# Kernel tuning notes

Hardware: AMD Instinct MI355X
Metric: run time of the kernel (lower is better)

The kernel has to match this reference:

```python
import jax, jax.numpy as jnp
import numpy as np

INPUT_DIM = 64
HIDDEN = 256
BATCH = 256
SEQ = 512
LN_EPS = 1e-5


def setup_inputs() -> dict:
    key = jax.random.key(0)
    ks = jax.random.split(key, 10)
    def lin(k, fan_in, fan_out):
        bound = 1.0 / np.sqrt(fan_in)
        kw, kb = jax.random.split(k)
        W = jax.random.uniform(kw, (fan_in, fan_out), jnp.float32, -bound, bound)
        b = jax.random.uniform(kb, (fan_out,), jnp.float32, -bound, bound)
        return W, b
    x = jax.random.normal(ks[0], (BATCH, SEQ, INPUT_DIM), jnp.float32)
    # layer 0: input_dim -> hidden
    Wz0, bz0 = lin(ks[1], INPUT_DIM + HIDDEN, 3 * HIDDEN)
    Wc0, bc0 = lin(ks[2], INPUT_DIM + HIDDEN, HIDDEN)
    # layer 1: hidden -> hidden
    Wz1, bz1 = lin(ks[3], HIDDEN + HIDDEN, 3 * HIDDEN)
    Wc1, bc1 = lin(ks[4], HIDDEN + HIDDEN, HIDDEN)
    ln_gamma = jnp.ones((HIDDEN,), jnp.float32)
    ln_beta = jnp.zeros((HIDDEN,), jnp.float32)
    return {"x": x, "Wz0": Wz0, "bz0": bz0, "Wc0": Wc0, "bc0": bc0,
            "Wz1": Wz1, "bz1": bz1, "Wc1": Wc1, "bc1": bc1,
            "ln_gamma": ln_gamma, "ln_beta": ln_beta}


def _gru_cell(h, x_t, Wz, bz, Wc, bc):
    # combined = [h, x]  (hidden first, as in the torch code)
    combined = jnp.concatenate([h, x_t], axis=-1)
    gates = combined @ Wz + bz  # (B, 3H); third chunk is unused (as in source)
    z = jax.nn.sigmoid(gates[:, :HIDDEN])
    r = jax.nn.sigmoid(gates[:, HIDDEN:2 * HIDDEN])
    reset_combined = jnp.concatenate([r * h, x_t], axis=-1)
    h_tilde = jnp.tanh(reset_combined @ Wc + bc)
    return (1.0 - z) * h + z * h_tilde


def reference(x, Wz0, bz0, Wc0, bc0, Wz1, bz1, Wc1, bc1, ln_gamma, ln_beta):
    # sanitize: NaN -> 0, Inf -> sign * 10
    x = jnp.where(jnp.isnan(x), 0.0, x)
    x = jnp.where(jnp.isinf(x), jnp.sign(x) * 10.0, x)

    B = x.shape[0]
    h0 = jnp.zeros((B, HIDDEN), x.dtype)
    h1 = jnp.zeros((B, HIDDEN), x.dtype)

    def step(carry, x_t):
        h0, h1 = carry
        h0 = _gru_cell(h0, x_t, Wz0, bz0, Wc0, bc0)
        h1 = _gru_cell(h1, h0, Wz1, bz1, Wc1, bc1)
        return (h0, h1), None

    xs = jnp.swapaxes(x, 0, 1)  # (seq, batch, input_dim)
    (h0, h1), _ = jax.lax.scan(step, (h0, h1), xs)

    # LayerNorm on final top-layer hidden state
    mean = jnp.mean(h1, axis=-1, keepdims=True)
    var = jnp.var(h1, axis=-1, keepdims=True)
    enc = (h1 - mean) * jax.lax.rsqrt(var + LN_EPS) * ln_gamma + ln_beta
    return enc
```

## Files before the change

kernel.cpp:

```cpp
#include <hip/hip_runtime.h>


#define SEQL 512
#define CH 8
#define NCH 64
#define DEPTH 4

#define RB0  1310720u
#define GSTR 1048576u
#define CTRB (RB0 + 16u * GSTR)

typedef __bf16 bf16x8 __attribute__((ext_vector_type(8)));
typedef float f32x4 __attribute__((ext_vector_type(4)));
typedef unsigned int u32x4 __attribute__((ext_vector_type(4)));
typedef unsigned long long u64;

__device__ __forceinline__ unsigned short f2bf(float f) {
  unsigned int u = __builtin_bit_cast(unsigned int, f);
  u += 0x7fffu + ((u >> 16) & 1u);
  return (unsigned short)(u >> 16);
}
__device__ __forceinline__ float bf2f(unsigned short u) {
  unsigned int v = ((unsigned int)u) << 16;
  return __builtin_bit_cast(float, v);
}
__device__ __forceinline__ float sigm(float x) { return 1.0f / (1.0f + __expf(-x)); }
__device__ __forceinline__ float tanh_(float x) { return 1.0f - 2.0f / (__expf(2.0f * x) + 1.0f); }
__device__ __forceinline__ float sanit(float v) {
  if (!(v == v)) return 0.f;
  if (isinf(v)) return v > 0.f ? 10.f : -10.f;
  return v;
}

__device__ __forceinline__ void st8(u64* p, u64 v) {
  __hip_atomic_store(p, v, __ATOMIC_RELAXED, __HIP_MEMORY_SCOPE_AGENT);
}

__device__ __forceinline__ void ld_frame8(const unsigned short* base, int lane, u32x4* c) {
  const char* p0 = (const char*)base + lane * 16;
  const char* p4 = p0 + 4096;
  asm volatile(
      "global_load_dwordx4 %0, %8, off sc0 sc1\n\t"
      "global_load_dwordx4 %1, %8, off offset:1024 sc0 sc1\n\t"
      "global_load_dwordx4 %2, %8, off offset:2048 sc0 sc1\n\t"
      "global_load_dwordx4 %3, %8, off offset:3072 sc0 sc1\n\t"
      "global_load_dwordx4 %4, %9, off sc0 sc1\n\t"
      "global_load_dwordx4 %5, %9, off offset:1024 sc0 sc1\n\t"
      "global_load_dwordx4 %6, %9, off offset:2048 sc0 sc1\n\t"
      "global_load_dwordx4 %7, %9, off offset:3072 sc0 sc1\n\t"
      "s_waitcnt vmcnt(0)"
      : "=&v"(c[0]), "=&v"(c[1]), "=&v"(c[2]), "=&v"(c[3]),
        "=&v"(c[4]), "=&v"(c[5]), "=&v"(c[6]), "=&v"(c[7])
      : "v"(p0), "v"(p4)
      : "memory");
}
__device__ __forceinline__ void ld_part6(const unsigned short* pf, int wave, int lane,
                                         u64* z, u64* r, u64* c) {
  const char* p0 = (const char*)pf + ((2 * wave) * 64 + lane) * 8;
  const char* p1 = p0 + 8192;
  const char* p2 = p0 + 16384;
  asm volatile(
      "global_load_dwordx2 %0, %6, off sc0 sc1\n\t"
      "global_load_dwordx2 %1, %6, off offset:512 sc0 sc1\n\t"
      "global_load_dwordx2 %2, %7, off sc0 sc1\n\t"
      "global_load_dwordx2 %3, %7, off offset:512 sc0 sc1\n\t"
      "global_load_dwordx2 %4, %8, off sc0 sc1\n\t"
      "global_load_dwordx2 %5, %8, off offset:512 sc0 sc1\n\t"
      "s_waitcnt vmcnt(0)"
      : "=&v"(z[0]), "=&v"(z[1]), "=&v"(r[0]), "=&v"(r[1]),
        "=&v"(c[0]), "=&v"(c[1])
      : "v"(p0), "v"(p1), "v"(p2)
      : "memory");
}

__global__ __launch_bounds__(256) void prep_weights(
    const float* __restrict__ Wz0, const float* __restrict__ Wc0,
    const float* __restrict__ Wz1, const float* __restrict__ Wc1,
    unsigned short* __restrict__ ws) {
  int idx = blockIdx.x * 256 + threadIdx.x;
  const float* W;
  int stride, KT, base;
  if (idx < 163840)      { W = Wz0; stride = 768; KT = 10; base = 0; }
  else if (idx < 245760) { W = Wc0; stride = 256; KT = 10; base = 163840; idx -= 163840; }
  else if (idx < 507904) { W = Wz1; stride = 768; KT = 16; base = 245760; idx -= 245760; }
  else                   { W = Wc1; stride = 256; KT = 16; base = 507904; idx -= 507904; }
  int tile = idx >> 9;
  int t = idx & 511;
  int nt = tile / KT;
  int kt = tile - nt * KT;
  int n15 = t & 15;
  int klocal = t >> 4;
  int k = (kt << 5) + klocal;
  int n = (nt << 4) + n15;
  int lane = ((klocal >> 3) << 4) | n15;
  int j = klocal & 7;
  ws[base + (tile << 9) + (lane << 3) + j] = f2bf(W[k * stride + n]);
}

__device__ __forceinline__ void waitge(int* p, int v, int tid) {
  __syncthreads();
  if (tid == 0) {
    long it = 0;
    while (__hip_atomic_load(p, __ATOMIC_RELAXED, __HIP_MEMORY_SCOPE_AGENT) < v) {
      __builtin_amdgcn_s_sleep(1);
      if (++it > (1L << 24)) break;
    }
  }
  __syncthreads();
}
__device__ __forceinline__ void publish(int* p, int v, int tid) {
  asm volatile("s_waitcnt vmcnt(0)" ::: "memory");
  __syncthreads();
  if (tid == 0) __hip_atomic_store(p, v, __ATOMIC_RELAXED, __HIP_MEMORY_SCOPE_AGENT);
}

#define DLOC(c) ((((c) >> 5) << 9) + (((((c) >> 3) & 3) << 4) + (quad << 2)) * 8 + ((c) & 7))
#define MFMA(a, b, c) __builtin_amdgcn_mfma_f32_16x16x32_bf16((a), (b), (c), 0, 0, 0)

union UB  { u32x4 q; bf16x8 v; };
union UB8 { u64 q; ushort4 s; };

__global__ __launch_bounds__(512, 2) void gru_pipe(
    const float* __restrict__ x,
    const float* __restrict__ bz0, const float* __restrict__ bc0,
    const float* __restrict__ bz1, const float* __restrict__ bc1,
    const float* __restrict__ gamma, const float* __restrict__ beta,
    const unsigned short* __restrict__ wsw,
    unsigned short* __restrict__ gws,
    float* __restrict__ out) {
  __shared__ __align__(16) unsigned short lds[75776];
  const int tid  = threadIdx.x;
  const int wave = tid >> 6;
  const int lane = tid & 63;
  const int l15  = lane & 15;
  const int quad = lane >> 4;
  const int stage = blockIdx.x >> 4;
  const int g     = blockIdx.x & 15;
  const int row0  = g << 4;

  const bf16x8* __restrict__ wsv = (const bf16x8*)wsw;
  unsigned short* ringh = gws + (RB0 >> 1) + (size_t)g * (GSTR >> 1);
  unsigned short* ringp = ringh + 131072;
  int* ctr = (int*)((char*)gws + CTRB) + g * 16;

  if (stage == 0) {
    unsigned short* h0f  = lds;
    unsigned short* rh0f = lds + 4096;
    unsigned short* xf   = lds + 8192;
    unsigned short* xw   = lds + 10240;
    unsigned short* cw0  = lds + 59392;
    for (int u = tid; u < 6144; u += 512) {
      int flat = u << 3, ti = flat >> 9, q = flat & 511, srct;
      if (ti < 64) srct = (ti >> 1) * 10 + 8 + (ti & 1);
      else         srct = 320 + ((ti - 64) >> 1) * 10 + 8 + (ti & 1);
      *(uint4*)(xw + flat) = *(const uint4*)(wsw + srct * 512 + q);
    }
    for (int u = tid; u < 2048; u += 512) {
      int flat = u << 3, ti = flat >> 9, q = flat & 511;
      int srct = 320 + (ti >> 1) * 10 + 6 + (ti & 1);
      *(uint4*)(cw0 + flat) = *(const uint4*)(wsw + srct * 512 + q);
    }
    for (int i = tid; i < 4096; i += 512) h0f[i] = 0;

    bf16x8 pz[2][8], pr[2][8], pc[2][6];
#pragma unroll
    for (int j = 0; j < 2; ++j) {
      const int zt = 2 * wave + j;
#pragma unroll
      for (int k = 0; k < 8; ++k) {
        pz[j][k] = wsv[(zt * 10 + k) * 64 + lane];
        pr[j][k] = wsv[((16 + zt) * 10 + k) * 64 + lane];
      }
#pragma unroll
      for (int k = 0; k < 6; ++k)
        pc[j][k] = wsv[(320 + zt * 10 + k) * 64 + lane];
    }
#pragma unroll
    for (int j = 0; j < 2; ++j) {
#pragma unroll
      for (int k = 0; k < 8; ++k)
        asm volatile("" : "+a"(pz[j][k]), "+a"(pr[j][k]));
#pragma unroll
      for (int k = 0; k < 6; ++k)
        asm volatile("" : "+a"(pc[j][k]));
    }

    float bzz[2], bzr[2], bcc[2];
    int dloc[2];
#pragma unroll
    for (int j = 0; j < 2; ++j) {
      const int col = 32 * wave + 16 * j + l15;
      bzz[j] = bz0[col]; bzr[j] = bz0[256 + col]; bcc[j] = bc0[col];
      dloc[j] = DLOC(col);
    }
    f32x4 h0s[2] = {{0,0,0,0},{0,0,0,0}};

    const int xrow = (tid >> 4) & 15, c4 = (tid & 15) << 2;
    const float* xp = x + (size_t)(row0 + xrow) * (SEQL * 64) + c4;
    const int xbase = ((c4 >> 5) << 9) + ((((c4 >> 3) & 3) << 4) + xrow) * 8 + (c4 & 7);
    if (tid < 256) {
      float4 xv = *(const float4*)xp;
      xf[xbase] = f2bf(sanit(xv.x)); xf[xbase + 1] = f2bf(sanit(xv.y));
      xf[xbase + 2] = f2bf(sanit(xv.z)); xf[xbase + 3] = f2bf(sanit(xv.w));
    }
    __syncthreads();

    for (int ch = 0; ch < NCH; ++ch) {
      if (ch >= DEPTH) waitge(ctr + 2, ch - (DEPTH - 1), tid);
      unsigned short* slot = ringh + (ch & (DEPTH - 1)) * (CH * 4096);
      for (int s = 0; s < CH; ++s) {
        const int t = (ch << 3) + s;
        if (s > 0) {
          u64* dst = (u64*)(slot + (s - 1) * 4096);
          const u64* src = (const u64*)h0f;
#pragma unroll
          for (int q = 0; q < 2; ++q) st8(dst + tid + 512 * q, src[tid + 512 * q]);
        }
        const unsigned short* xb = xf + ((t & 1) << 10);
        const bool havex = (t + 1 < SEQL) && (tid < 256);
        float4 xn;
        if (havex) xn = *(const float4*)(xp + (t + 1) * 64);

        f32x4 za[2], ra[2];
#pragma unroll
        for (int j = 0; j < 2; ++j) { za[j] = {bzz[j],bzz[j],bzz[j],bzz[j]}; ra[j] = {bzr[j],bzr[j],bzr[j],bzr[j]}; }
#pragma unroll
        for (int k = 0; k < 8; ++k) {
          bf16x8 a = *(const bf16x8*)(h0f + (k << 9) + (lane << 3));
#pragma unroll
          for (int j = 0; j < 2; ++j) { za[j] = MFMA(a, pz[j][k], za[j]); ra[j] = MFMA(a, pr[j][k], ra[j]); }
        }
#pragma unroll
        for (int k = 0; k < 2; ++k) {
          bf16x8 a = *(const bf16x8*)(xb + (k << 9) + (lane << 3));
#pragma unroll
          for (int j = 0; j < 2; ++j) {
            bf16x8 bz_ = *(const bf16x8*)(xw + ((((2 * wave + j) << 1) | k) << 9) + (lane << 3));
            bf16x8 br_ = *(const bf16x8*)(xw + ((((16 + 2 * wave + j) << 1) | k) << 9) + (lane << 3));
            za[j] = MFMA(a, bz_, za[j]); ra[j] = MFMA(a, br_, ra[j]);
          }
        }
        float zg[2][4];
#pragma unroll
        for (int j = 0; j < 2; ++j)
#pragma unroll
          for (int i = 0; i < 4; ++i) {
            zg[j][i] = sigm(za[j][i]);
            rh0f[dloc[j] + i * 8] = f2bf(sigm(ra[j][i]) * h0s[j][i]);
          }
        __syncthreads();

        f32x4 ca[2];
#pragma unroll
        for (int j = 0; j < 2; ++j) ca[j] = {bcc[j],bcc[j],bcc[j],bcc[j]};
#pragma unroll
        for (int k = 0; k < 6; ++k) {
          bf16x8 a = *(const bf16x8*)(rh0f + (k << 9) + (lane << 3));
#pragma unroll
          for (int j = 0; j < 2; ++j) ca[j] = MFMA(a, pc[j][k], ca[j]);
        }
#pragma unroll
        for (int kk = 0; kk < 2; ++kk) {
          bf16x8 a = *(const bf16x8*)(rh0f + ((6 + kk) << 9) + (lane << 3));
#pragma unroll
          for (int j = 0; j < 2; ++j) {
            bf16x8 bc_ = *(const bf16x8*)(cw0 + ((((2 * wave + j) << 1) | kk) << 9) + (lane << 3));
            ca[j] = MFMA(a, bc_, ca[j]);
          }
        }
#pragma unroll
        for (int k = 0; k < 2; ++k) {
          bf16x8 a = *(const bf16x8*)(xb + (k << 9) + (lane << 3));
#pragma unroll
          for (int j = 0; j < 2; ++j) {
            bf16x8 bc_ = *(const bf16x8*)(xw + 32768 + ((((2 * wave + j) << 1) | k) << 9) + (lane << 3));
            ca[j] = MFMA(a, bc_, ca[j]);
          }
        }
#pragma unroll
        for (int j = 0; j < 2; ++j)
#pragma unroll
          for (int i = 0; i < 4; ++i) {
            float ht = tanh_(ca[j][i]);
            float hn = h0s[j][i] + zg[j][i] * (ht - h0s[j][i]);
            h0s[j][i] = hn;
            h0f[dloc[j] + i * 8] = f2bf(hn);
          }
        if (havex) {
          unsigned short* xb1 = xf + (((t + 1) & 1) << 10);
          xb1[xbase] = f2bf(sanit(xn.x)); xb1[xbase + 1] = f2bf(sanit(xn.y));
          xb1[xbase + 2] = f2bf(sanit(xn.z)); xb1[xbase + 3] = f2bf(sanit(xn.w));
        }
        __syncthreads();
      }
      {
        u64* dst = (u64*)(slot + 7 * 4096);
        const u64* src = (const u64*)h0f;
#pragma unroll
        for (int q = 0; q < 2; ++q) st8(dst + tid + 512 * q, src[tid + 512 * q]);
      }
      publish(ctr + 0, ch + 1, tid);
    }
  } else if (stage == 1) {
    unsigned short* cwB = lds;
    for (int u = tid; u < 2048; u += 512) {
      int flat = u << 3, ti = flat >> 9, q = flat & 511;
      int srct = 992 + (ti >> 1) * 16 + 14 + (ti & 1);
      *(uint4*)(cwB + flat) = *(const uint4*)(wsw + srct * 512 + q);
    }
    __syncthreads();

    bf16x8 p1[2][8], p2[2][8], p3[2][6];
#pragma unroll
    for (int j = 0; j < 2; ++j) {
      const int nt = 2 * wave + j;
#pragma unroll
      for (int k = 0; k < 8; ++k) {
        p1[j][k] = wsv[(480 + nt * 16 + 8 + k) * 64 + lane];
        p2[j][k] = wsv[(480 + (16 + nt) * 16 + 8 + k) * 64 + lane];
      }
#pragma unroll
      for (int k = 0; k < 6; ++k)
        p3[j][k] = wsv[(992 + nt * 16 + 8 + k) * 64 + lane];
    }
#pragma unroll
    for (int j = 0; j < 2; ++j) {
#pragma unroll
      for (int k = 0; k < 8; ++k)
        asm volatile("" : "+a"(p1[j][k]), "+a"(p2[j][k]));
#pragma unroll
      for (int k = 0; k < 6; ++k)
        asm volatile("" : "+a"(p3[j][k]));
    }
    float b1[2], b2[2], b3[2];
#pragma unroll
    for (int j = 0; j < 2; ++j) {
      const int col = 32 * wave + 16 * j + l15;
      b1[j] = bz1[col]; b2[j] = bz1[256 + col]; b3[j] = bc1[col];
    }
    for (int ch = 0; ch < NCH; ++ch) {
      waitge(ctr + 0, ch + 1, tid);
      if (ch >= DEPTH) waitge(ctr + 3, ch - (DEPTH - 1), tid);
      const unsigned short* hslot = ringh + (ch & (DEPTH - 1)) * (CH * 4096);
      unsigned short* pslot = ringp + (ch & (DEPTH - 1)) * (CH * 12288);
      for (int s = 0; s < CH; ++s) {
        u32x4 cf[8];
        ld_frame8(hslot + s * 4096, lane, cf);
        f32x4 za[2] = {{0,0,0,0},{0,0,0,0}};
        f32x4 ra[2] = {{0,0,0,0},{0,0,0,0}};
        f32x4 ca[2] = {{0,0,0,0},{0,0,0,0}};
#pragma unroll
        for (int k = 0; k < 8; ++k) {
          UB ub; ub.q = cf[k];
          bf16x8 a = ub.v;
#pragma unroll
          for (int j = 0; j < 2; ++j) {
            za[j] = MFMA(a, p1[j][k], za[j]);
            ra[j] = MFMA(a, p2[j][k], ra[j]);
            if (k < 6) ca[j] = MFMA(a, p3[j][k], ca[j]);
          }
        }
#pragma unroll
        for (int kk = 0; kk < 2; ++kk) {
          UB ub; ub.q = cf[6 + kk];
          bf16x8 a = ub.v;
#pragma unroll
          for (int j = 0; j < 2; ++j) {
            bf16x8 bc_ = *(const bf16x8*)(cwB + ((((2 * wave + j) << 1) | kk) << 9) + (lane << 3));
            ca[j] = MFMA(a, bc_, ca[j]);
          }
        }
        u64* pf = (u64*)(pslot + s * 12288);
#pragma unroll
        for (int j = 0; j < 2; ++j) {
          ushort4 vz, vr, vc;
          vz.x = f2bf(za[j][0] + b1[j]); vz.y = f2bf(za[j][1] + b1[j]);
          vz.z = f2bf(za[j][2] + b1[j]); vz.w = f2bf(za[j][3] + b1[j]);
          vr.x = f2bf(ra[j][0] + b2[j]); vr.y = f2bf(ra[j][1] + b2[j]);
          vr.z = f2bf(ra[j][2] + b2[j]); vr.w = f2bf(ra[j][3] + b2[j]);
          vc.x = f2bf(ca[j][0] + b3[j]); vc.y = f2bf(ca[j][1] + b3[j]);
          vc.z = f2bf(ca[j][2] + b3[j]); vc.w = f2bf(ca[j][3] + b3[j]);
          st8(pf + (2 * wave + j) * 64 + lane,      __builtin_bit_cast(u64, vz));
          st8(pf + (16 + 2 * wave + j) * 64 + lane, __builtin_bit_cast(u64, vr));
          st8(pf + (32 + 2 * wave + j) * 64 + lane, __builtin_bit_cast(u64, vc));
        }
      }
      publish(ctr + 1, ch + 1, tid);
      if (tid == 0)
        __hip_atomic_store(ctr + 2, ch + 1, __ATOMIC_RELAXED, __HIP_MEMORY_SCOPE_AGENT);
    }
  } else {
    unsigned short* h1f  = lds;
    unsigned short* rh1f = lds + 4096;
    unsigned short* cwC  = lds + 8192;
    for (int u = tid; u < 2048; u += 512) {
      int flat = u << 3, ti = flat >> 9, q = flat & 511;
      int srct = 992 + (ti >> 1) * 16 + 6 + (ti & 1);
      *(uint4*)(cwC + flat) = *(const uint4*)(wsw + srct * 512 + q);
    }
    bf16x8 q1[2][8], q2[2][8], q3[2][6];
#pragma unroll
    for (int j = 0; j < 2; ++j) {
      const int nt = 2 * wave + j;
#pragma unroll
      for (int k = 0; k < 8; ++k) {
        q1[j][k] = wsv[(480 + nt * 16 + k) * 64 + lane];
        q2[j][k] = wsv[(480 + (16 + nt) * 16 + k) * 64 + lane];
      }
#pragma unroll
      for (int k = 0; k < 6; ++k)
        q3[j][k] = wsv[(992 + nt * 16 + k) * 64 + lane];
    }
#pragma unroll
    for (int j = 0; j < 2; ++j) {
#pragma unroll
      for (int k = 0; k < 8; ++k)
        asm volatile("" : "+a"(q1[j][k]), "+a"(q2[j][k]));
#pragma unroll
      for (int k = 0; k < 6; ++k)
        asm volatile("" : "+a"(q3[j][k]));
    }
    for (int i = tid; i < 4096; i += 512) h1f[i] = 0;
    int dloc[2];
#pragma unroll
    for (int j = 0; j < 2; ++j) dloc[j] = DLOC(32 * wave + 16 * j + l15);
    f32x4 h1s[2] = {{0,0,0,0},{0,0,0,0}};
    __syncthreads();

    for (int ch = 0; ch < NCH; ++ch) {
      waitge(ctr + 1, ch + 1, tid);
      const unsigned short* pslot = ringp + (ch & (DEPTH - 1)) * (CH * 12288);
      for (int s = 0; s < CH; ++s) {
        u64 zq[2], rq[2], cq[2];
        ld_part6(pslot + s * 12288, wave, lane, zq, rq, cq);
        f32x4 za[2] = {{0,0,0,0},{0,0,0,0}};
        f32x4 ra[2] = {{0,0,0,0},{0,0,0,0}};
#pragma unroll
        for (int k = 0; k < 8; ++k) {
          bf16x8 a = *(const bf16x8*)(h1f + (k << 9) + (lane << 3));
#pragma unroll
          for (int j = 0; j < 2; ++j) { za[j] = MFMA(a, q1[j][k], za[j]); ra[j] = MFMA(a, q2[j][k], ra[j]); }
        }
        float zg[2][4];
#pragma unroll
        for (int j = 0; j < 2; ++j) {
          UB8 uz, ur; uz.q = zq[j]; ur.q = rq[j];
#pragma unroll
          for (int i = 0; i < 4; ++i) {
            zg[j][i] = sigm(za[j][i] + bf2f(((const unsigned short*)&uz.s)[i]));
            float r = sigm(ra[j][i] + bf2f(((const unsigned short*)&ur.s)[i]));
            rh1f[dloc[j] + i * 8] = f2bf(r * h1s[j][i]);
          }
        }
        __syncthreads();

        f32x4 ca[2] = {{0,0,0,0},{0,0,0,0}};
#pragma unroll
        for (int k = 0; k < 6; ++k) {
          bf16x8 a = *(const bf16x8*)(rh1f + (k << 9) + (lane << 3));
#pragma unroll
          for (int j = 0; j < 2; ++j) ca[j] = MFMA(a, q3[j][k], ca[j]);
        }
#pragma unroll
        for (int kk = 0; kk < 2; ++kk) {
          bf16x8 a = *(const bf16x8*)(rh1f + ((6 + kk) << 9) + (lane << 3));
#pragma unroll
          for (int j = 0; j < 2; ++j) {
            bf16x8 bc_ = *(const bf16x8*)(cwC + ((((2 * wave + j) << 1) | kk) << 9) + (lane << 3));
            ca[j] = MFMA(a, bc_, ca[j]);
          }
        }
#pragma unroll
        for (int j = 0; j < 2; ++j) {
          UB8 uc; uc.q = cq[j];
#pragma unroll
          for (int i = 0; i < 4; ++i) {
            float ht = tanh_(ca[j][i] + bf2f(((const unsigned short*)&uc.s)[i]));
            float hn = h1s[j][i] + zg[j][i] * (ht - h1s[j][i]);
            h1s[j][i] = hn;
            h1f[dloc[j] + i * 8] = f2bf(hn);
          }
        }
        __syncthreads();
      }
      publish(ctr + 3, ch + 1, tid);
    }

    float* h1buf = (float*)lds;
#pragma unroll
    for (int j = 0; j < 2; ++j)
#pragma unroll
      for (int i = 0; i < 4; ++i)
        h1buf[(quad * 4 + i) * 256 + 32 * wave + 16 * j + l15] = h1s[j][i];
    __syncthreads();

    if (tid < 256) {
      const int r = tid >> 4, cl = tid & 15;
      float v[16], s = 0.f, sq = 0.f;
#pragma unroll
      for (int jj = 0; jj < 16; ++jj) {
        v[jj] = h1buf[r * 256 + cl + (jj << 4)];
        s += v[jj]; sq += v[jj] * v[jj];
      }
#pragma unroll
      for (int off = 8; off > 0; off >>= 1) {
        s  += __shfl_xor(s, off);
        sq += __shfl_xor(sq, off);
      }
      const float mean = s * (1.f / 256.f);
      const float var  = sq * (1.f / 256.f) - mean * mean;
      const float rstd = rsqrtf(var + 1e-5f);
      float* op = out + (size_t)(row0 + r) * 256;
#pragma unroll
      for (int jj = 0; jj < 16; ++jj) {
        const int c = cl + (jj << 4);
        op[c] = (v[jj] - mean) * rstd * gamma[c] + beta[c];
      }
    }
  }
}

extern "C" void kernel_launch(void* const* d_in, const int* in_sizes, int n_in,
                              void* d_out, int out_size, void* d_ws, size_t ws_size,
                              hipStream_t stream) {
  const float* x     = (const float*)d_in[0];
  const float* Wz0   = (const float*)d_in[1];
  const float* bz0   = (const float*)d_in[2];
  const float* Wc0   = (const float*)d_in[3];
  const float* bc0   = (const float*)d_in[4];
  const float* Wz1   = (const float*)d_in[5];
  const float* bz1   = (const float*)d_in[6];
  const float* Wc1   = (const float*)d_in[7];
  const float* bc1   = (const float*)d_in[8];
  const float* gamma = (const float*)d_in[9];
  const float* beta  = (const float*)d_in[10];
  unsigned short* ws = (unsigned short*)d_ws;
  float* out = (float*)d_out;

  hipMemsetAsync((char*)d_ws + CTRB, 0, 1024, stream);
  hipLaunchKernelGGL(prep_weights, dim3(2496), dim3(256), 0, stream, Wz0, Wc0, Wz1, Wc1, ws);
  hipLaunchKernelGGL(gru_pipe, dim3(48), dim3(512), 0, stream,
                     x, bz0, bc0, bz1, bc1, gamma, beta, ws, ws, out);
}
```

Baseline: 2.331 ms.

## Prefetch next-step gate partials in layer-1 recurrence and widen ring stores

In the layer-1 recurrent stage, the global loads of the precomputed z/r/c partials for step s+1 are now issued before the candidate matmul of step s and waited on afterwards. This hides their latency behind compute instead of stalling at the start of each step. The h0 frame copy to the ring now uses one 16-byte store per thread instead of two 8-byte atomic stores. The partial-gate bf16 packing uses the hardware v_cvt_pk_bf16_f32 instruction in place of manual rounding. The prefetch uses double register sets and a split wait, which raises register pressure slightly.

```diff
diff --git a/kernel.cpp b/kernel.cpp
--- a/kernel.cpp
+++ b/kernel.cpp
@@ -23,6 +23,11 @@
 __device__ __forceinline__ float bf2f(unsigned short u) {
   unsigned int v = ((unsigned int)u) << 16;
   return __builtin_bit_cast(float, v);
+}
+__device__ __forceinline__ unsigned int cvtpk(float lo, float hi) {
+  unsigned int r;
+  asm("v_cvt_pk_bf16_f32 %0, %1, %2" : "=v"(r) : "v"(lo), "v"(hi));
+  return r;
 }
 __device__ __forceinline__ float sigm(float x) { return 1.0f / (1.0f + __expf(-x)); }
 __device__ __forceinline__ float tanh_(float x) { return 1.0f - 2.0f / (__expf(2.0f * x) + 1.0f); }
@@ -34,6 +39,9 @@
 
 __device__ __forceinline__ void st8(u64* p, u64 v) {
   __hip_atomic_store(p, v, __ATOMIC_RELAXED, __HIP_MEMORY_SCOPE_AGENT);
+}
+__device__ __forceinline__ void st16(void* p, u32x4 v) {
+  asm volatile("global_store_dwordx4 %0, %1, off sc0 sc1" :: "v"(p), "v"(v) : "memory");
 }
 
 __device__ __forceinline__ void ld_frame8(const unsigned short* base, int lane, u32x4* c) {
@@ -71,6 +79,28 @@
         "=&v"(c[0]), "=&v"(c[1])
       : "v"(p0), "v"(p1), "v"(p2)
       : "memory");
+}
+__device__ __forceinline__ void ld_part6_issue(const unsigned short* pf, int wave, int lane,
+                                               u64* z, u64* r, u64* c) {
+  const char* p0 = (const char*)pf + ((2 * wave) * 64 + lane) * 8;
+  const char* p1 = p0 + 8192;
+  const char* p2 = p0 + 16384;
+  asm volatile(
+      "global_load_dwordx2 %0, %6, off sc0 sc1\n\t"
+      "global_load_dwordx2 %1, %6, off offset:512 sc0 sc1\n\t"
+      "global_load_dwordx2 %2, %7, off sc0 sc1\n\t"
+      "global_load_dwordx2 %3, %7, off offset:512 sc0 sc1\n\t"
+      "global_load_dwordx2 %4, %8, off sc0 sc1\n\t"
+      "global_load_dwordx2 %5, %8, off offset:512 sc0 sc1"
+      : "=&v"(z[0]), "=&v"(z[1]), "=&v"(r[0]), "=&v"(r[1]),
+        "=&v"(c[0]), "=&v"(c[1])
+      : "v"(p0), "v"(p1), "v"(p2)
+      : "memory");
+}
+__device__ __forceinline__ void wait_vm0_6(u64* z, u64* r, u64* c) {
+  asm volatile("s_waitcnt vmcnt(0)"
+      : "+v"(z[0]), "+v"(z[1]), "+v"(r[0]), "+v"(r[1]), "+v"(c[0]), "+v"(c[1])
+      :: "memory");
 }
 
 __global__ __launch_bounds__(256) void prep_weights(
@@ -119,6 +149,7 @@
 
 union UB  { u32x4 q; bf16x8 v; };
 union UB8 { u64 q; ushort4 s; };
+union UPK { u64 q; uint2 u; };
 
 __global__ __launch_bounds__(512, 2) void gru_pipe(
     const float* __restrict__ x,
@@ -211,10 +242,8 @@
       for (int s = 0; s < CH; ++s) {
         const int t = (ch << 3) + s;
         if (s > 0) {
-          u64* dst = (u64*)(slot + (s - 1) * 4096);
-          const u64* src = (const u64*)h0f;
-#pragma unroll
-          for (int q = 0; q < 2; ++q) st8(dst + tid + 512 * q, src[tid + 512 * q]);
+          u32x4 fv = *(const u32x4*)((const char*)h0f + 16 * tid);
+          st16((char*)(slot + (s - 1) * 4096) + 16 * tid, fv);
         }
         const unsigned short* xb = xf + ((t & 1) << 10);
         const bool havex = (t + 1 < SEQL) && (tid < 256);
@@ -294,10 +323,8 @@
         __syncthreads();
       }
       {
-        u64* dst = (u64*)(slot + 7 * 4096);
-        const u64* src = (const u64*)h0f;
-#pragma unroll
-        for (int q = 0; q < 2; ++q) st8(dst + tid + 512 * q, src[tid + 512 * q]);
+        u32x4 fv = *(const u32x4*)((const char*)h0f + 16 * tid);
+        st16((char*)(slot + 7 * 4096) + 16 * tid, fv);
       }
       publish(ctr + 0, ch + 1, tid);
     }
@@ -373,16 +400,16 @@
         u64* pf = (u64*)(pslot + s * 12288);
 #pragma unroll
         for (int j = 0; j < 2; ++j) {
-          ushort4 vz, vr, vc;
-          vz.x = f2bf(za[j][0] + b1[j]); vz.y = f2bf(za[j][1] + b1[j]);
-          vz.z = f2bf(za[j][2] + b1[j]); vz.w = f2bf(za[j][3] + b1[j]);
-          vr.x = f2bf(ra[j][0] + b2[j]); vr.y = f2bf(ra[j][1] + b2[j]);
-          vr.z = f2bf(ra[j][2] + b2[j]); vr.w = f2bf(ra[j][3] + b2[j]);
-          vc.x = f2bf(ca[j][0] + b3[j]); vc.y = f2bf(ca[j][1] + b3[j]);
-          vc.z = f2bf(ca[j][2] + b3[j]); vc.w = f2bf(ca[j][3] + b3[j]);
-          st8(pf + (2 * wave + j) * 64 + lane,      __builtin_bit_cast(u64, vz));
-          st8(pf + (16 + 2 * wave + j) * 64 + lane, __builtin_bit_cast(u64, vr));
-          st8(pf + (32 + 2 * wave + j) * 64 + lane, __builtin_bit_cast(u64, vc));
+          UPK vz, vr, vc;
+          vz.u.x = cvtpk(za[j][0] + b1[j], za[j][1] + b1[j]);
+          vz.u.y = cvtpk(za[j][2] + b1[j], za[j][3] + b1[j]);
+          vr.u.x = cvtpk(ra[j][0] + b2[j], ra[j][1] + b2[j]);
+          vr.u.y = cvtpk(ra[j][2] + b2[j], ra[j][3] + b2[j]);
+          vc.u.x = cvtpk(ca[j][0] + b3[j], ca[j][1] + b3[j]);
+          vc.u.y = cvtpk(ca[j][2] + b3[j], ca[j][3] + b3[j]);
+          st8(pf + (2 * wave + j) * 64 + lane,      vz.q);
+          st8(pf + (16 + 2 * wave + j) * 64 + lane, vr.q);
+          st8(pf + (32 + 2 * wave + j) * 64 + lane, vc.q);
         }
       }
       publish(ctr + 1, ch + 1, tid);
@@ -427,61 +454,77 @@
     f32x4 h1s[2] = {{0,0,0,0},{0,0,0,0}};
     __syncthreads();
 
+    auto cph1 = [&](u64* zq, u64* rq, float zg[2][4]) {
+      f32x4 za[2] = {{0,0,0,0},{0,0,0,0}};
+      f32x4 ra[2] = {{0,0,0,0},{0,0,0,0}};
+#pragma unroll
+      for (int k = 0; k < 8; ++k) {
+        bf16x8 a = *(const bf16x8*)(h1f + (k << 9) + (lane << 3));
+#pragma unroll
+        for (int j = 0; j < 2; ++j) { za[j] = MFMA(a, q1[j][k], za[j]); ra[j] = MFMA(a, q2[j][k], ra[j]); }
+      }
+#pragma unroll
+      for (int j = 0; j < 2; ++j) {
+        UB8 uz, ur; uz.q = zq[j]; ur.q = rq[j];
+#pragma unroll
+        for (int i = 0; i < 4; ++i) {
+          zg[j][i] = sigm(za[j][i] + bf2f(((const unsigned short*)&uz.s)[i]));
+          float r = sigm(ra[j][i] + bf2f(((const unsigned short*)&ur.s)[i]));
+          rh1f[dloc[j] + i * 8] = f2bf(r * h1s[j][i]);
+        }
+      }
+    };
+    auto cph2 = [&](u64* cq, float zg[2][4]) {
+      f32x4 ca[2] = {{0,0,0,0},{0,0,0,0}};
+#pragma unroll
+      for (int k = 0; k < 6; ++k) {
+        bf16x8 a = *(const bf16x8*)(rh1f + (k << 9) + (lane << 3));
+#pragma unroll
+        for (int j = 0; j < 2; ++j) ca[j] = MFMA(a, q3[j][k], ca[j]);
+      }
+#pragma unroll
+      for (int kk = 0; kk < 2; ++kk) {
+        bf16x8 a = *(const bf16x8*)(rh1f + ((6 + kk) << 9) + (lane << 3));
+#pragma unroll
+        for (int j = 0; j < 2; ++j) {
+          bf16x8 bc_ = *(const bf16x8*)(cwC + ((((2 * wave + j) << 1) | kk) << 9) + (lane << 3));
+          ca[j] = MFMA(a, bc_, ca[j]);
+        }
+      }
+#pragma unroll
+      for (int j = 0; j < 2; ++j) {
+        UB8 uc; uc.q = cq[j];
+#pragma unroll
+        for (int i = 0; i < 4; ++i) {
+          float ht = tanh_(ca[j][i] + bf2f(((const unsigned short*)&uc.s)[i]));
+          float hn = h1s[j][i] + zg[j][i] * (ht - h1s[j][i]);
+          h1s[j][i] = hn;
+          h1f[dloc[j] + i * 8] = f2bf(hn);
+        }
+      }
+    };
+
     for (int ch = 0; ch < NCH; ++ch) {
       waitge(ctr + 1, ch + 1, tid);
       const unsigned short* pslot = ringp + (ch & (DEPTH - 1)) * (CH * 12288);
-      for (int s = 0; s < CH; ++s) {
-        u64 zq[2], rq[2], cq[2];
-        ld_part6(pslot + s * 12288, wave, lane, zq, rq, cq);
-        f32x4 za[2] = {{0,0,0,0},{0,0,0,0}};
-        f32x4 ra[2] = {{0,0,0,0},{0,0,0,0}};
-#pragma unroll
-        for (int k = 0; k < 8; ++k) {
-          bf16x8 a = *(const bf16x8*)(h1f + (k << 9) + (lane << 3));
-#pragma unroll
-          for (int j = 0; j < 2; ++j) { za[j] = MFMA(a, q1[j][k], za[j]); ra[j] = MFMA(a, q2[j][k], ra[j]); }
-        }
-        float zg[2][4];
-#pragma unroll
-        for (int j = 0; j < 2; ++j) {
-          UB8 uz, ur; uz.q = zq[j]; ur.q = rq[j];
-#pragma unroll
-          for (int i = 0; i < 4; ++i) {
-            zg[j][i] = sigm(za[j][i] + bf2f(((const unsigned short*)&uz.s)[i]));
-            float r = sigm(ra[j][i] + bf2f(((const unsigned short*)&ur.s)[i]));
-            rh1f[dloc[j] + i * 8] = f2bf(r * h1s[j][i]);
-          }
-        }
+      u64 zqA[2], rqA[2], cqA[2], zqB[2], rqB[2], cqB[2];
+      ld_part6(pslot, wave, lane, zqA, rqA, cqA);
+#pragma unroll
+      for (int s2 = 0; s2 < 4; ++s2) {
+        const int s = 2 * s2;
+        float zg1[2][4], zg2[2][4];
+        cph1(zqA, rqA, zg1);
         __syncthreads();
-
-        f32x4 ca[2] = {{0,0,0,0},{0,0,0,0}};
-#pragma unroll
-        for (int k = 0; k < 6; ++k) {
-          bf16x8 a = *(const bf16x8*)(rh1f + (k << 9) + (lane << 3));
-#pragma unroll
-          for (int j = 0; j < 2; ++j) ca[j] = MFMA(a, q3[j][k], ca[j]);
-        }
-#pragma unroll
-        for (int kk = 0; kk < 2; ++kk) {
-          bf16x8 a = *(const bf16x8*)(rh1f + ((6 + kk) << 9) + (lane << 3));
-#pragma unroll
-          for (int j = 0; j < 2; ++j) {
-            bf16x8 bc_ = *(const bf16x8*)(cwC + ((((2 * wave + j) << 1) | kk) << 9) + (lane << 3));
-            ca[j] = MFMA(a, bc_, ca[j]);
-          }
-        }
-#pragma unroll
-        for (int j = 0; j < 2; ++j) {
-          UB8 uc; uc.q = cq[j];
-#pragma unroll
-          for (int i = 0; i < 4; ++i) {
-            float ht = tanh_(ca[j][i] + bf2f(((const unsigned short*)&uc.s)[i]));
-            float hn = h1s[j][i] + zg[j][i] * (ht - h1s[j][i]);
-            h1s[j][i] = hn;
-            h1f[dloc[j] + i * 8] = f2bf(hn);
-          }
-        }
+        ld_part6_issue(pslot + (s + 1) * 12288, wave, lane, zqB, rqB, cqB);
+        cph2(cqA, zg1);
         __syncthreads();
+        wait_vm0_6(zqB, rqB, cqB);
+        cph1(zqB, rqB, zg2);
+        __syncthreads();
+        if (s2 < 3) ld_part6_issue(pslot + (s + 2) * 12288, wave, lane, zqA, rqA, cqA);
+        cph2(cqB, zg2);
+        __syncthreads();
+        if (s2 < 3) wait_vm0_6(zqA, rqA, cqA);
       }
       publish(ctr + 3, ch + 1, tid);
     }
```

Measured after the change: 2.714 ms. 16.4% more time.

## Double block size so each wave computes one 16-column tile

Applied to the files above, without the earlier changes.

The GRU pipeline kernel now launches 1024 threads per block instead of 512, and each wave owns a single 16-column output tile instead of two. The per-wave MFMA chains, register-resident weight fragments, bias and state arrays and global partial loads are all halved, and the cooperative LDS loops are restrided. The aim is to shorten the serial per-timestep critical path in this latency-bound recurrence by spreading it over twice as many waves. The cost is more waves joining each block barrier, plus tighter per-thread register limits under the new launch bounds.

```diff
diff --git a/kernel.cpp b/kernel.cpp
--- a/kernel.cpp
+++ b/kernel.cpp
@@ -54,21 +54,17 @@
       : "v"(p0), "v"(p4)
       : "memory");
 }
-__device__ __forceinline__ void ld_part6(const unsigned short* pf, int wave, int lane,
+__device__ __forceinline__ void ld_part3(const unsigned short* pf, int w, int lane,
                                          u64* z, u64* r, u64* c) {
-  const char* p0 = (const char*)pf + ((2 * wave) * 64 + lane) * 8;
+  const char* p0 = (const char*)pf + (w * 64 + lane) * 8;
   const char* p1 = p0 + 8192;
   const char* p2 = p0 + 16384;
   asm volatile(
-      "global_load_dwordx2 %0, %6, off sc0 sc1\n\t"
-      "global_load_dwordx2 %1, %6, off offset:512 sc0 sc1\n\t"
-      "global_load_dwordx2 %2, %7, off sc0 sc1\n\t"
-      "global_load_dwordx2 %3, %7, off offset:512 sc0 sc1\n\t"
-      "global_load_dwordx2 %4, %8, off sc0 sc1\n\t"
-      "global_load_dwordx2 %5, %8, off offset:512 sc0 sc1\n\t"
+      "global_load_dwordx2 %0, %3, off sc0 sc1\n\t"
+      "global_load_dwordx2 %1, %4, off sc0 sc1\n\t"
+      "global_load_dwordx2 %2, %5, off sc0 sc1\n\t"
       "s_waitcnt vmcnt(0)"
-      : "=&v"(z[0]), "=&v"(z[1]), "=&v"(r[0]), "=&v"(r[1]),
-        "=&v"(c[0]), "=&v"(c[1])
+      : "=&v"(*z), "=&v"(*r), "=&v"(*c)
       : "v"(p0), "v"(p1), "v"(p2)
       : "memory");
 }
@@ -120,7 +116,7 @@
 union UB  { u32x4 q; bf16x8 v; };
 union UB8 { u64 q; ushort4 s; };
 
-__global__ __launch_bounds__(512, 2) void gru_pipe(
+__global__ __launch_bounds__(1024, 4) void gru_pipe(
     const float* __restrict__ x,
     const float* __restrict__ bz0, const float* __restrict__ bc0,
     const float* __restrict__ bz1, const float* __restrict__ bc1,
@@ -130,7 +126,7 @@
     float* __restrict__ out) {
   __shared__ __align__(16) unsigned short lds[75776];
   const int tid  = threadIdx.x;
-  const int wave = tid >> 6;
+  const int w    = tid >> 6;
   const int lane = tid & 63;
   const int l15  = lane & 15;
   const int quad = lane >> 4;
@@ -149,51 +145,39 @@
     unsigned short* xf   = lds + 8192;
     unsigned short* xw   = lds + 10240;
     unsigned short* cw0  = lds + 59392;
-    for (int u = tid; u < 6144; u += 512) {
+    for (int u = tid; u < 6144; u += 1024) {
       int flat = u << 3, ti = flat >> 9, q = flat & 511, srct;
       if (ti < 64) srct = (ti >> 1) * 10 + 8 + (ti & 1);
       else         srct = 320 + ((ti - 64) >> 1) * 10 + 8 + (ti & 1);
       *(uint4*)(xw + flat) = *(const uint4*)(wsw + srct * 512 + q);
     }
-    for (int u = tid; u < 2048; u += 512) {
+    for (int u = tid; u < 2048; u += 1024) {
       int flat = u << 3, ti = flat >> 9, q = flat & 511;
       int srct = 320 + (ti >> 1) * 10 + 6 + (ti & 1);
       *(uint4*)(cw0 + flat) = *(const uint4*)(wsw + srct * 512 + q);
     }
-    for (int i = tid; i < 4096; i += 512) h0f[i] = 0;
-
-    bf16x8 pz[2][8], pr[2][8], pc[2][6];
-#pragma unroll
-    for (int j = 0; j < 2; ++j) {
-      const int zt = 2 * wave + j;
-#pragma unroll
-      for (int k = 0; k < 8; ++k) {
-        pz[j][k] = wsv[(zt * 10 + k) * 64 + lane];
-        pr[j][k] = wsv[((16 + zt) * 10 + k) * 64 + lane];
-      }
-#pragma unroll
-      for (int k = 0; k < 6; ++k)
-        pc[j][k] = wsv[(320 + zt * 10 + k) * 64 + lane];
-    }
-#pragma unroll
-    for (int j = 0; j < 2; ++j) {
-#pragma unroll
-      for (int k = 0; k < 8; ++k)
-        asm volatile("" : "+a"(pz[j][k]), "+a"(pr[j][k]));
-#pragma unroll
-      for (int k = 0; k < 6; ++k)
-        asm volatile("" : "+a"(pc[j][k]));
-    }
-
-    float bzz[2], bzr[2], bcc[2];
-    int dloc[2];
-#pragma unroll
-    for (int j = 0; j < 2; ++j) {
-      const int col = 32 * wave + 16 * j + l15;
-      bzz[j] = bz0[col]; bzr[j] = bz0[256 + col]; bcc[j] = bc0[col];
-      dloc[j] = DLOC(col);
-    }
-    f32x4 h0s[2] = {{0,0,0,0},{0,0,0,0}};
+    for (int i = tid; i < 4096; i += 1024) h0f[i] = 0;
+
+    bf16x8 pz[8], pr[8], pc[6];
+#pragma unroll
+    for (int k = 0; k < 8; ++k) {
+      pz[k] = wsv[(w * 10 + k) * 64 + lane];
+      pr[k] = wsv[((16 + w) * 10 + k) * 64 + lane];
+    }
+#pragma unroll
+    for (int k = 0; k < 6; ++k)
+      pc[k] = wsv[(320 + w * 10 + k) * 64 + lane];
+#pragma unroll
+    for (int k = 0; k < 8; ++k)
+      asm volatile("" : "+a"(pz[k]), "+a"(pr[k]));
+#pragma unroll
+    for (int k = 0; k < 6; ++k)
+      asm volatile("" : "+a"(pc[k]));
+
+    const int col = 16 * w + l15;
+    const float bzz = bz0[col], bzr = bz0[256 + col], bcc = bc0[col];
+    const int dloc = DLOC(col);
+    f32x4 h0s = {0, 0, 0, 0};
 
     const int xrow = (tid >> 4) & 15, c4 = (tid & 15) << 2;
     const float* xp = x + (size_t)(row0 + xrow) * (SEQL * 64) + c4;
@@ -213,79 +197,60 @@
         if (s > 0) {
           u64* dst = (u64*)(slot + (s - 1) * 4096);
           const u64* src = (const u64*)h0f;
-#pragma unroll
-          for (int q = 0; q < 2; ++q) st8(dst + tid + 512 * q, src[tid + 512 * q]);
+          st8(dst + tid, src[tid]);
         }
         const unsigned short* xb = xf + ((t & 1) << 10);
         const bool havex = (t + 1 < SEQL) && (tid < 256);
         float4 xn;
         if (havex) xn = *(const float4*)(xp + (t + 1) * 64);
 
-        f32x4 za[2], ra[2];
-#pragma unroll
-        for (int j = 0; j < 2; ++j) { za[j] = {bzz[j],bzz[j],bzz[j],bzz[j]}; ra[j] = {bzr[j],bzr[j],bzr[j],bzr[j]}; }
+        f32x4 za = {bzz, bzz, bzz, bzz};
+        f32x4 ra = {bzr, bzr, bzr, bzr};
 #pragma unroll
         for (int k = 0; k < 8; ++k) {
           bf16x8 a = *(const bf16x8*)(h0f + (k << 9) + (lane << 3));
-#pragma unroll
-          for (int j = 0; j < 2; ++j) { za[j] = MFMA(a, pz[j][k], za[j]); ra[j] = MFMA(a, pr[j][k], ra[j]); }
+          za = MFMA(a, pz[k], za); ra = MFMA(a, pr[k], ra);
         }
 #pragma unroll
         for (int k = 0; k < 2; ++k) {
           bf16x8 a = *(const bf16x8*)(xb + (k << 9) + (lane << 3));
-#pragma unroll
-          for (int j = 0; j < 2; ++j) {
-            bf16x8 bz_ = *(const bf16x8*)(xw + ((((2 * wave + j) << 1) | k) << 9) + (lane << 3));
-            bf16x8 br_ = *(const bf16x8*)(xw + ((((16 + 2 * wave + j) << 1) | k) << 9) + (lane << 3));
-            za[j] = MFMA(a, bz_, za[j]); ra[j] = MFMA(a, br_, ra[j]);
-          }
-        }
-        float zg[2][4];
-#pragma unroll
-        for (int j = 0; j < 2; ++j)
-#pragma unroll
-          for (int i = 0; i < 4; ++i) {
-            zg[j][i] = sigm(za[j][i]);
-            rh0f[dloc[j] + i * 8] = f2bf(sigm(ra[j][i]) * h0s[j][i]);
-          }
+          bf16x8 bz_ = *(const bf16x8*)(xw + (((w << 1) | k) << 9) + (lane << 3));
+          bf16x8 br_ = *(const bf16x8*)(xw + ((((16 + w) << 1) | k) << 9) + (lane << 3));
+          za = MFMA(a, bz_, za); ra = MFMA(a, br_, ra);
+        }
+        float zg[4];
+#pragma unroll
+        for (int i = 0; i < 4; ++i) {
+          zg[i] = sigm(za[i]);
+          rh0f[dloc + i * 8] = f2bf(sigm(ra[i]) * h0s[i]);
+        }
         __syncthreads();
 
-        f32x4 ca[2];
-#pragma unroll
-        for (int j = 0; j < 2; ++j) ca[j] = {bcc[j],bcc[j],bcc[j],bcc[j]};
+        f32x4 ca = {bcc, bcc, bcc, bcc};
 #pragma unroll
         for (int k = 0; k < 6; ++k) {
           bf16x8 a = *(const bf16x8*)(rh0f + (k << 9) + (lane << 3));
-#pragma unroll
-          for (int j = 0; j < 2; ++j) ca[j] = MFMA(a, pc[j][k], ca[j]);
+          ca = MFMA(a, pc[k], ca);
         }
 #pragma unroll
         for (int kk = 0; kk < 2; ++kk) {
           bf16x8 a = *(const bf16x8*)(rh0f + ((6 + kk) << 9) + (lane << 3));
-#pragma unroll
-          for (int j = 0; j < 2; ++j) {
-            bf16x8 bc_ = *(const bf16x8*)(cw0 + ((((2 * wave + j) << 1) | kk) << 9) + (lane << 3));
-            ca[j] = MFMA(a, bc_, ca[j]);
-          }
+          bf16x8 bc_ = *(const bf16x8*)(cw0 + (((w << 1) | kk) << 9) + (lane << 3));
+          ca = MFMA(a, bc_, ca);
         }
 #pragma unroll
         for (int k = 0; k < 2; ++k) {
           bf16x8 a = *(const bf16x8*)(xb + (k << 9) + (lane << 3));
-#pragma unroll
-          for (int j = 0; j < 2; ++j) {
-            bf16x8 bc_ = *(const bf16x8*)(xw + 32768 + ((((2 * wave + j) << 1) | k) << 9) + (lane << 3));
-            ca[j] = MFMA(a, bc_, ca[j]);
-          }
-        }
-#pragma unroll
-        for (int j = 0; j < 2; ++j)
-#pragma unroll
-          for (int i = 0; i < 4; ++i) {
-            float ht = tanh_(ca[j][i]);
-            float hn = h0s[j][i] + zg[j][i] * (ht - h0s[j][i]);
-            h0s[j][i] = hn;
-            h0f[dloc[j] + i * 8] = f2bf(hn);
-          }
+          bf16x8 bc_ = *(const bf16x8*)(xw + 32768 + (((w << 1) | k) << 9) + (lane << 3));
+          ca = MFMA(a, bc_, ca);
+        }
+#pragma unroll
+        for (int i = 0; i < 4; ++i) {
+          float ht = tanh_(ca[i]);
+          float hn = h0s[i] + zg[i] * (ht - h0s[i]);
+          h0s[i] = hn;
+          h0f[dloc + i * 8] = f2bf(hn);
+        }
         if (havex) {
           unsigned short* xb1 = xf + (((t + 1) & 1) << 10);
           xb1[xbase] = f2bf(sanit(xn.x)); xb1[xbase + 1] = f2bf(sanit(xn.y));
@@ -296,48 +261,37 @@
       {
         u64* dst = (u64*)(slot + 7 * 4096);
         const u64* src = (const u64*)h0f;
-#pragma unroll
-        for (int q = 0; q < 2; ++q) st8(dst + tid + 512 * q, src[tid + 512 * q]);
+        st8(dst + tid, src[tid]);
       }
       publish(ctr + 0, ch + 1, tid);
     }
   } else if (stage == 1) {
     unsigned short* cwB = lds;
-    for (int u = tid; u < 2048; u += 512) {
+    for (int u = tid; u < 2048; u += 1024) {
       int flat = u << 3, ti = flat >> 9, q = flat & 511;
       int srct = 992 + (ti >> 1) * 16 + 14 + (ti & 1);
       *(uint4*)(cwB + flat) = *(const uint4*)(wsw + srct * 512 + q);
     }
     __syncthreads();
 
-    bf16x8 p1[2][8], p2[2][8], p3[2][6];
-#pragma unroll
-    for (int j = 0; j < 2; ++j) {
-      const int nt = 2 * wave + j;
-#pragma unroll
-      for (int k = 0; k < 8; ++k) {
-        p1[j][k] = wsv[(480 + nt * 16 + 8 + k) * 64 + lane];
-        p2[j][k] = wsv[(480 + (16 + nt) * 16 + 8 + k) * 64 + lane];
-      }
-#pragma unroll
-      for (int k = 0; k < 6; ++k)
-        p3[j][k] = wsv[(992 + nt * 16 + 8 + k) * 64 + lane];
-    }
-#pragma unroll
-    for (int j = 0; j < 2; ++j) {
-#pragma unroll
-      for (int k = 0; k < 8; ++k)
-        asm volatile("" : "+a"(p1[j][k]), "+a"(p2[j][k]));
-#pragma unroll
-      for (int k = 0; k < 6; ++k)
-        asm volatile("" : "+a"(p3[j][k]));
-    }
-    float b1[2], b2[2], b3[2];
-#pragma unroll
-    for (int j = 0; j < 2; ++j) {
-      const int col = 32 * wave + 16 * j + l15;
-      b1[j] = bz1[col]; b2[j] = bz1[256 + col]; b3[j] = bc1[col];
-    }
+    bf16x8 p1[8], p2[8], p3[6];
+#pragma unroll
+    for (int k = 0; k < 8; ++k) {
+      p1[k] = wsv[(480 + w * 16 + 8 + k) * 64 + lane];
+      p2[k] = wsv[(480 + (16 + w) * 16 + 8 + k) * 64 + lane];
+    }
+#pragma unroll
+    for (int k = 0; k < 6; ++k)
+      p3[k] = wsv[(992 + w * 16 + 8 + k) * 64 + lane];
+#pragma unroll
+    for (int k = 0; k < 8; ++k)
+      asm volatile("" : "+a"(p1[k]), "+a"(p2[k]));
+#pragma unroll
+    for (int k = 0; k < 6; ++k)
+      asm volatile("" : "+a"(p3[k]));
+    const int col = 16 * w + l15;
+    const float b1 = bz1[col], b2 = bz1[256 + col], b3 = bc1[col];
+
     for (int ch = 0; ch < NCH; ++ch) {
       waitge(ctr + 0, ch + 1, tid);
       if (ch >= DEPTH) waitge(ctr + 3, ch - (DEPTH - 1), tid);
@@ -346,44 +300,33 @@
       for (int s = 0; s < CH; ++s) {
         u32x4 cf[8];
         ld_frame8(hslot + s * 4096, lane, cf);
-        f32x4 za[2] = {{0,0,0,0},{0,0,0,0}};
-        f32x4 ra[2] = {{0,0,0,0},{0,0,0,0}};
-        f32x4 ca[2] = {{0,0,0,0},{0,0,0,0}};
+        f32x4 za = {0, 0, 0, 0}, ra = {0, 0, 0, 0}, ca = {0, 0, 0, 0};
 #pragma unroll
         for (int k = 0; k < 8; ++k) {
           UB ub; ub.q = cf[k];
           bf16x8 a = ub.v;
-#pragma unroll
-          for (int j = 0; j < 2; ++j) {
-            za[j] = MFMA(a, p1[j][k], za[j]);
-            ra[j] = MFMA(a, p2[j][k], ra[j]);
-            if (k < 6) ca[j] = MFMA(a, p3[j][k], ca[j]);
-          }
+          za = MFMA(a, p1[k], za);
+          ra = MFMA(a, p2[k], ra);
+          if (k < 6) ca = MFMA(a, p3[k], ca);
         }
 #pragma unroll
         for (int kk = 0; kk < 2; ++kk) {
           UB ub; ub.q = cf[6 + kk];
           bf16x8 a = ub.v;
-#pragma unroll
-          for (int j = 0; j < 2; ++j) {
-            bf16x8 bc_ = *(const bf16x8*)(cwB + ((((2 * wave + j) << 1) | kk) << 9) + (lane << 3));
-            ca[j] = MFMA(a, bc_, ca[j]);
-          }
+          bf16x8 bc_ = *(const bf16x8*)(cwB + (((w << 1) | kk) << 9) + (lane << 3));
+          ca = MFMA(a, bc_, ca);
         }
         u64* pf = (u64*)(pslot + s * 12288);
-#pragma unroll
-        for (int j = 0; j < 2; ++j) {
-          ushort4 vz, vr, vc;
-          vz.x = f2bf(za[j][0] + b1[j]); vz.y = f2bf(za[j][1] + b1[j]);
-          vz.z = f2bf(za[j][2] + b1[j]); vz.w = f2bf(za[j][3] + b1[j]);
-          vr.x = f2bf(ra[j][0] + b2[j]); vr.y = f2bf(ra[j][1] + b2[j]);
-          vr.z = f2bf(ra[j][2] + b2[j]); vr.w = f2bf(ra[j][3] + b2[j]);
-          vc.x = f2bf(ca[j][0] + b3[j]); vc.y = f2bf(ca[j][1] + b3[j]);
-          vc.z = f2bf(ca[j][2] + b3[j]); vc.w = f2bf(ca[j][3] + b3[j]);
-          st8(pf + (2 * wave + j) * 64 + lane,      __builtin_bit_cast(u64, vz));
-          st8(pf + (16 + 2 * wave + j) * 64 + lane, __builtin_bit_cast(u64, vr));
-          st8(pf + (32 + 2 * wave + j) * 64 + lane, __builtin_bit_cast(u64, vc));
-        }
+        ushort4 vz, vr, vc;
+        vz.x = f2bf(za[0] + b1); vz.y = f2bf(za[1] + b1);
+        vz.z = f2bf(za[2] + b1); vz.w = f2bf(za[3] + b1);
+        vr.x = f2bf(ra[0] + b2); vr.y = f2bf(ra[1] + b2);
+        vr.z = f2bf(ra[2] + b2); vr.w = f2bf(ra[3] + b2);
+        vc.x = f2bf(ca[0] + b3); vc.y = f2bf(ca[1] + b3);
+        vc.z = f2bf(ca[2] + b3); vc.w = f2bf(ca[3] + b3);
+        st8(pf + w * 64 + lane,        __builtin_bit_cast(u64, vz));
+        st8(pf + (16 + w) * 64 + lane, __builtin_bit_cast(u64, vr));
+        st8(pf + (32 + w) * 64 + lane, __builtin_bit_cast(u64, vc));
       }
       publish(ctr + 1, ch + 1, tid);
       if (tid == 0)
@@ -393,94 +336,78 @@
     unsigned short* h1f  = lds;
     unsigned short* rh1f = lds + 4096;
     unsigned short* cwC  = lds + 8192;
-    for (int u = tid; u < 2048; u += 512) {
+    for (int u = tid; u < 2048; u += 1024) {
       int flat = u << 3, ti = flat >> 9, q = flat & 511;
       int srct = 992 + (ti >> 1) * 16 + 6 + (ti & 1);
       *(uint4*)(cwC + flat) = *(const uint4*)(wsw + srct * 512 + q);
     }
-    bf16x8 q1[2][8], q2[2][8], q3[2][6];
-#pragma unroll
-    for (int j = 0; j < 2; ++j) {
-      const int nt = 2 * wave + j;
-#pragma unroll
-      for (int k = 0; k < 8; ++k) {
-        q1[j][k] = wsv[(480 + nt * 16 + k) * 64 + lane];
-        q2[j][k] = wsv[(480 + (16 + nt) * 16 + k) * 64 + lane];
-      }
-#pragma unroll
-      for (int k = 0; k < 6; ++k)
-        q3[j][k] = wsv[(992 + nt * 16 + k) * 64 + lane];
-    }
-#pragma unroll
-    for (int j = 0; j < 2; ++j) {
-#pragma unroll
-      for (int k = 0; k < 8; ++k)
-        asm volatile("" : "+a"(q1[j][k]), "+a"(q2[j][k]));
-#pragma unroll
-      for (int k = 0; k < 6; ++k)
-        asm volatile("" : "+a"(q3[j][k]));
-    }
-    for (int i = tid; i < 4096; i += 512) h1f[i] = 0;
-    int dloc[2];
-#pragma unroll
-    for (int j = 0; j < 2; ++j) dloc[j] = DLOC(32 * wave + 16 * j + l15);
-    f32x4 h1s[2] = {{0,0,0,0},{0,0,0,0}};
+    bf16x8 q1[8], q2[8], q3[6];
+#pragma unroll
+    for (int k = 0; k < 8; ++k) {
+      q1[k] = wsv[(480 + w * 16 + k) * 64 + lane];
+      q2[k] = wsv[(480 + (16 + w) * 16 + k) * 64 + lane];
+    }
+#pragma unroll
+    for (int k = 0; k < 6; ++k)
+      q3[k] = wsv[(992 + w * 16 + k) * 64 + lane];
+#pragma unroll
+    for (int k = 0; k < 8; ++k)
+      asm volatile("" : "+a"(q1[k]), "+a"(q2[k]));
+#pragma unroll
+    for (int k = 0; k < 6; ++k)
+      asm volatile("" : "+a"(q3[k]));
+    for (int i = tid; i < 4096; i += 1024) h1f[i] = 0;
+    const int col = 16 * w + l15;
+    const int dloc = DLOC(col);
+    f32x4 h1s = {0, 0, 0, 0};
     __syncthreads();
 
     for (int ch = 0; ch < NCH; ++ch) {
       waitge(ctr + 1, ch + 1, tid);
       const unsigned short* pslot = ringp + (ch & (DEPTH - 1)) * (CH * 12288);
       for (int s = 0; s < CH; ++s) {
-        u64 zq[2], rq[2], cq[2];
-        ld_part6(pslot + s * 12288, wave, lane, zq, rq, cq);
-        f32x4 za[2] = {{0,0,0,0},{0,0,0,0}};
-        f32x4 ra[2] = {{0,0,0,0},{0,0,0,0}};
+        u64 zq, rq, cq;
+        ld_part3(pslot + s * 12288, w, lane, &zq, &rq, &cq);
+        f32x4 za = {0, 0, 0, 0}, ra = {0, 0, 0, 0};
 #pragma unroll
         for (int k = 0; k < 8; ++k) {
           bf16x8 a = *(const bf16x8*)(h1f + (k << 9) + (lane << 3));
-#pragma unroll
-          for (int j = 0; j < 2; ++j) { za[j] = MFMA(a, q1[j][k], za[j]); ra[j] = MFMA(a, q2[j][k], ra[j]); }
-        }
-        float zg[2][4];
-#pragma unroll
-        for (int j = 0; j < 2; ++j) {
-          UB8 uz, ur; uz.q = zq[j]; ur.q = rq[j];
+          za = MFMA(a, q1[k], za); ra = MFMA(a, q2[k], ra);
+        }
+        float zg[4];
+        {
+          UB8 uz, ur; uz.q = zq; ur.q = rq;
 #pragma unroll
           for (int i = 0; i < 4; ++i) {
-            zg[j][i] = sigm(za[j][i] + bf2f(((const unsigned short*)&uz.s)[i]));
-            float r = sigm(ra[j][i] + bf2f(((const unsigned short*)&ur.s)[i]));
-            rh1f[dloc[j] + i * 8] = f2bf(r * h1s[j][i]);
+            zg[i] = sigm(za[i] + bf2f(((const unsigned short*)&uz.s)[i]));
+            float r = sigm(ra[i] + bf2f(((const unsigned short*)&ur.s)[i]));
+            rh1f[dloc + i * 8] = f2bf(r * h1s[i]);
           }
         }
         __syncthreads();
 
-        f32x4 ca[2] = {{0,0,0,0},{0,0,0,0}};
+        f32x4 ca = {0, 0, 0, 0};
 #pragma unroll
         for (int k = 0; k < 6; ++k) {
           bf16x8 a = *(const bf16x8*)(rh1f + (k << 9) + (lane << 3));
-#pragma unroll
-          for (int j = 0; j < 2; ++j) ca[j] = MFMA(a, q3[j][k], ca[j]);
+          ca = MFMA(a, q3[k], ca);
         }
 #pragma unroll
         for (int kk = 0; kk < 2; ++kk) {
           bf16x8 a = *(const bf16x8*)(rh1f + ((6 + kk) << 9) + (lane << 3));
-#pragma unroll
-          for (int j = 0; j < 2; ++j) {
-            bf16x8 bc_ = *(const bf16x8*)(cwC + ((((2 * wave + j) << 1) | kk) << 9) + (lane << 3));
-            ca[j] = MFMA(a, bc_, ca[j]);
+          bf16x8 bc_ = *(const bf16x8*)(cwC + (((w << 1) | kk) << 9) + (lane << 3));
+          ca = MFMA(a, bc_, ca);
+        }
+        {
+          UB8 uc; uc.q = cq;
+#pragma unroll
+          for (int i = 0; i < 4; ++i) {
+            float ht = tanh_(ca[i] + bf2f(((const unsigned short*)&uc.s)[i]));
+            float hn = h1s[i] + zg[i] * (ht - h1s[i]);
+            h1s[i] = hn;
+            h1f[dloc + i * 8] = f2bf(hn);
           }
         }
-#pragma unroll
-        for (int j = 0; j < 2; ++j) {
-          UB8 uc; uc.q = cq[j];
-#pragma unroll
-          for (int i = 0; i < 4; ++i) {
-            float ht = tanh_(ca[j][i] + bf2f(((const unsigned short*)&uc.s)[i]));
-            float hn = h1s[j][i] + zg[j][i] * (ht - h1s[j][i]);
-            h1s[j][i] = hn;
-            h1f[dloc[j] + i * 8] = f2bf(hn);
-          }
-        }
         __syncthreads();
       }
       publish(ctr + 3, ch + 1, tid);
@@ -488,10 +415,8 @@
 
     float* h1buf = (float*)lds;
 #pragma unroll
-    for (int j = 0; j < 2; ++j)
-#pragma unroll
-      for (int i = 0; i < 4; ++i)
-        h1buf[(quad * 4 + i) * 256 + 32 * wave + 16 * j + l15] = h1s[j][i];
+    for (int i = 0; i < 4; ++i)
+      h1buf[(quad * 4 + i) * 256 + 16 * w + l15] = h1s[i];
     __syncthreads();
 
     if (tid < 256) {
@@ -539,6 +464,6 @@
 
   hipMemsetAsync((char*)d_ws + CTRB, 0, 1024, stream);
   hipLaunchKernelGGL(prep_weights, dim3(2496), dim3(256), 0, stream, Wz0, Wc0, Wz1, Wc1, ws);
-  hipLaunchKernelGGL(gru_pipe, dim3(48), dim3(512), 0, stream,
+  hipLaunchKernelGGL(gru_pipe, dim3(48), dim3(1024), 0, stream,
                      x, bz0, bc0, bz1, bc1, gamma, beta, ws, ws, out);
 }
```

After: 2.723 ms. 1.17x slower.
